# Performance work log

Hardware: AMD Instinct MI355X
Metric: run time of the kernel (lower is better)

Reference implementation:

```python
import jax, jax.numpy as jnp
import numpy as np

D_MODEL = 1024
N_HEAD = 16
HEAD_DIM = D_MODEL // N_HEAD
N_POS = 4096
K_PROJ = 256  # self.k is hardcoded to 256 in the module
BATCH = 4


def setup_inputs() -> dict:
    key = jax.random.key(0)
    ks = jax.random.split(key, 11)
    s = 1.0 / np.sqrt(D_MODEL)
    return {
        "x": jax.random.normal(ks[0], (BATCH, N_POS, D_MODEL), jnp.float32),
        "Wq": jax.random.normal(ks[1], (D_MODEL, D_MODEL), jnp.float32) * s,
        "bq": jnp.zeros((D_MODEL,), jnp.float32),
        "Wk": jax.random.normal(ks[2], (D_MODEL, D_MODEL), jnp.float32) * s,
        "bk": jnp.zeros((D_MODEL,), jnp.float32),
        "Wv": jax.random.normal(ks[3], (D_MODEL, D_MODEL), jnp.float32) * s,
        "bv": jnp.zeros((D_MODEL,), jnp.float32),
        "E": jax.random.normal(ks[4], (K_PROJ, N_POS), jnp.float32),
        "F": jax.random.normal(ks[5], (K_PROJ, N_POS), jnp.float32),
        "Wo": jax.random.normal(ks[6], (D_MODEL, D_MODEL), jnp.float32) * s,
        "bo": jnp.zeros((D_MODEL,), jnp.float32),
    }


def reference(x, Wq, bq, Wk, bk, Wv, bv, E, F, Wo, bo):
    B, N, D = x.shape
    scale = jnp.sqrt(jnp.asarray(HEAD_DIM, x.dtype))
    # Q/K/V projections (nn.Linear applies x @ W.T + b)
    def proj(W, b):
        y = jnp.einsum('bnd,ed->bne', x, W) + b
        return y.reshape(B, N, N_HEAD, HEAD_DIM).transpose(0, 2, 1, 3)  # bhnd
    Q = proj(Wq, bq)
    K = proj(Wk, bk)
    V = proj(Wv, bv)
    # Linformer low-rank projections along sequence dim
    Kp = jnp.einsum('kn,bhnd->bhkd', E, K)
    Vp = jnp.einsum('kn,bhnd->bhkd', F, V)
    attn_score = jnp.einsum('bhnd,bhkd->bhnk', Q, Kp) / scale
    attn = jax.nn.softmax(attn_score, axis=-1)  # dropout is identity (drop_prob=0)
    out = jnp.einsum('bhnk,bhkd->bhnd', attn, Vp)
    out = out.transpose(0, 2, 1, 3).reshape(B, N, D)
    out = jnp.einsum('bnd,ed->bne', out, Wo) + bo
    return out, attn_score
```

## Files before the change

### kernel.cpp

```cpp
#include <hip/hip_runtime.h>

typedef _Float16 f16;
typedef __attribute__((ext_vector_type(8))) _Float16 f16x8;
typedef __attribute__((ext_vector_type(4))) _Float16 f16x4;
typedef __attribute__((ext_vector_type(4))) float f32x4;

typedef const __attribute__((address_space(1))) unsigned int* gas_ptr;
typedef __attribute__((address_space(3))) unsigned int* las_ptr;

__device__ __forceinline__ void gload16(const f16* g, f16* l) {
  __builtin_amdgcn_global_load_lds((gas_ptr)g, (las_ptr)l, 16, 0, 0);
}

template<int WM, int WN, bool OUT32>
__device__ __forceinline__ void gemm_core(
    const f16* __restrict__ A, int lda,
    const f16* __restrict__ B, int ldb,
    int kLen,
    f16* lsA, f16* lsB,
    float* __restrict__ C32, f16* __restrict__ C16, int ldc,
    float scale, const float* __restrict__ biasC, const float* __restrict__ biasR)
{
  constexpr int T   = WM * WN * 64;
  constexpr int nA  = (WM * 64 * 8) / T;
  constexpr int nB  = (WN * 64 * 8) / T;
  constexpr int RPI = T / 8;
  const int t    = threadIdx.x;
  const int lane = t & 63;
  const int wave = t >> 6;
  const int wm   = wave / WN;
  const int wn   = wave % WN;

  f32x4 acc[4][4];
  const f32x4 z4 = {0.f, 0.f, 0.f, 0.f};
#pragma unroll
  for (int i = 0; i < 4; ++i)
#pragma unroll
    for (int j = 0; j < 4; ++j) acc[i][j] = z4;

  const int r_ = t >> 3;
  const int c_ = (t & 7) * 8;
  const int ldsOff = (wave << 9);

  for (int kt = 0; kt < kLen; kt += 64) {
#pragma unroll
    for (int i = 0; i < nA; ++i) {
      const f16* g = A + (size_t)(i * RPI + r_) * lda + kt + c_;
      gload16(g, lsA + i * (T * 8) + ldsOff);
    }
#pragma unroll
    for (int i = 0; i < nB; ++i) {
      const f16* g = B + (size_t)(i * RPI + r_) * ldb + kt + c_;
      gload16(g, lsB + i * (T * 8) + ldsOff);
    }
    __syncthreads();
#pragma unroll
    for (int ks = 0; ks < 2; ++ks) {
      f16x8 af[4], bf[4];
#pragma unroll
      for (int i = 0; i < 4; ++i)
        af[i] = *(const f16x8*)&lsA[(wm * 64 + i * 16 + (lane & 15)) * 64 + ks * 32 + (lane >> 4) * 8];
#pragma unroll
      for (int j = 0; j < 4; ++j)
        bf[j] = *(const f16x8*)&lsB[(wn * 64 + j * 16 + (lane & 15)) * 64 + ks * 32 + (lane >> 4) * 8];
#pragma unroll
      for (int i = 0; i < 4; ++i)
#pragma unroll
        for (int j = 0; j < 4; ++j)
          acc[i][j] = __builtin_amdgcn_mfma_f32_16x16x32_f16(af[i], bf[j], acc[i][j], 0, 0, 0);
    }
    __syncthreads();
  }

  const int lc = lane & 15;
  const int lr = (lane >> 4) * 4;
#pragma unroll
  for (int j = 0; j < 4; ++j) {
    const int col = wn * 64 + j * 16 + lc;
    const float bC = biasC ? biasC[col] : 0.f;
#pragma unroll
    for (int i = 0; i < 4; ++i) {
      const int rbase = wm * 64 + i * 16 + lr;
#pragma unroll
      for (int r = 0; r < 4; ++r) {
        const int row = rbase + r;
        float v = acc[i][j][r] * scale + bC;
        if (biasR) v += biasR[row];
        if (OUT32) C32[(size_t)row * ldc + col] = v;
        else       C16[(size_t)row * ldc + col] = (f16)v;
      }
    }
  }
}

template<int WM, int WN, bool OUT32>
__global__ __launch_bounds__(WM * WN * 64) void k_gemm(
    const f16* A, int lda, const f16* B, int ldb, int kLen,
    float* C32, f16* C16, int ldc, float scale,
    const float* biasC, const float* biasR)
{
  __shared__ f16 lsA[WM * 64 * 64];
  __shared__ f16 lsB[WN * 64 * 64];
  const size_t rt = blockIdx.y, ct = blockIdx.x;
  gemm_core<WM, WN, OUT32>(
      A + rt * (WM * 64) * (size_t)lda, lda,
      B + ct * (WN * 64) * (size_t)ldb, ldb, kLen,
      lsA, lsB,
      OUT32 ? C32 + rt * (WM * 64) * (size_t)ldc + ct * (WN * 64) : nullptr,
      OUT32 ? nullptr : C16 + rt * (WM * 64) * (size_t)ldc + ct * (WN * 64), ldc,
      scale,
      biasC ? biasC + ct * (WN * 64) : nullptr,
      biasR ? biasR + rt * (WM * 64) : nullptr);
}

__global__ __launch_bounds__(256) void k_cast_xt(const float* __restrict__ x,
                                                 f16* __restrict__ Xf,
                                                 f16* __restrict__ XT)
{
  __shared__ f16 tile[64][68];
  const int b = blockIdx.z, bi = blockIdx.y, bj = blockIdx.x;
  const int r0 = threadIdx.x >> 4;
  const int c4 = (threadIdx.x & 15) * 4;
  const float* xb = x + ((size_t)b * 4096 + (size_t)bi * 64) * 1024 + bj * 64;
#pragma unroll
  for (int rr = 0; rr < 4; ++rr) {
    const int row = rr * 16 + r0;
    const float4 v = *(const float4*)(xb + (size_t)row * 1024 + c4);
    f16x4 h = {(f16)v.x, (f16)v.y, (f16)v.z, (f16)v.w};
    *(f16x4*)&tile[row][c4] = h;
    *(f16x4*)(Xf + ((size_t)b * 4096 + (size_t)bi * 64 + row) * 1024 + bj * 64 + c4) = h;
  }
  __syncthreads();
#pragma unroll
  for (int rr = 0; rr < 4; ++rr) {
    const int col = rr * 16 + r0;
    f16x4 h = {tile[c4 + 0][col], tile[c4 + 1][col], tile[c4 + 2][col], tile[c4 + 3][col]};
    *(f16x4*)(XT + ((size_t)b * 1024 + (size_t)bj * 64 + col) * 4096 + (size_t)bi * 64 + c4) = h;
  }
}

__global__ __launch_bounds__(256) void k_cast_w(
    const float* w0, const float* w1, const float* w2,
    const float* w3, const float* w4, const float* w5, f16* __restrict__ d)
{
  const size_t i = ((size_t)blockIdx.x * 256 + threadIdx.x) * 4;
  const int seg = (int)(i >> 20);
  const float* s = (seg == 0) ? w0 : (seg == 1) ? w1 : (seg == 2) ? w2
                 : (seg == 3) ? w3 : (seg == 4) ? w4 : w5;
  const float4 v = *(const float4*)(s + (i & 1048575));
  f16x4 o = {(f16)v.x, (f16)v.y, (f16)v.z, (f16)v.w};
  *(f16x4*)(d + i) = o;
}

__global__ __launch_bounds__(256) void k_rowsum(const float* __restrict__ E,
                                                const float* __restrict__ F,
                                                float* __restrict__ rs)
{
  const int r = blockIdx.x * 4 + (threadIdx.x >> 6);
  const int lane = threadIdx.x & 63;
  const float* src = (r < 256) ? (E + (size_t)r * 4096) : (F + (size_t)(r - 256) * 4096);
  float s = 0.f;
#pragma unroll
  for (int i = 0; i < 16; ++i) {
    const float4 v = *(const float4*)(src + i * 256 + lane * 4);
    s += v.x + v.y + v.z + v.w;
  }
#pragma unroll
  for (int o = 32; o; o >>= 1) s += __shfl_xor(s, o);
  if (lane == 0) rs[r] = s;
}

__global__ __launch_bounds__(256) void k_exfx(const f16* __restrict__ EF,
                                              const f16* __restrict__ XT,
                                              float* __restrict__ part)
{
  __shared__ f16 lsA[128 * 64];
  __shared__ f16 lsB[128 * 64];
  const int z = blockIdx.z; const int b = z & 3; const int s = z >> 2;
  const int rt = blockIdx.y, ct = blockIdx.x;
  const f16* A = EF + (size_t)rt * 128 * 4096 + s * 1024;
  const f16* B = XT + (size_t)b * 1024 * 4096 + (size_t)ct * 128 * 4096 + s * 1024;
  float* C = part + (size_t)z * (512 * 1024) + (size_t)rt * 128 * 1024 + ct * 128;
  gemm_core<2, 2, true>(A, 4096, B, 4096, 1024, lsA, lsB, C, nullptr, 1024, 1.f, nullptr, nullptr);
}

__global__ __launch_bounds__(256) void k_reduce2(const float* __restrict__ part,
                                                 f16* __restrict__ EXf)
{
  const size_t i = ((size_t)blockIdx.x * 256 + threadIdx.x) * 4;
  const size_t b = i >> 19;
  const size_t idx = i & 524287;
  const float4 a = *(const float4*)(part + (0 * 4 + b) * 524288 + idx);
  const float4 c1 = *(const float4*)(part + (1 * 4 + b) * 524288 + idx);
  const float4 c2 = *(const float4*)(part + (2 * 4 + b) * 524288 + idx);
  const float4 c3 = *(const float4*)(part + (3 * 4 + b) * 524288 + idx);
  f16x4 o = {(f16)(a.x + c1.x + c2.x + c3.x), (f16)(a.y + c1.y + c2.y + c3.y),
             (f16)(a.z + c1.z + c2.z + c3.z), (f16)(a.w + c1.w + c2.w + c3.w)};
  *(f16x4*)(EXf + i) = o;
}

__global__ __launch_bounds__(256) void k_kpvp(const f16* __restrict__ EXf,
                                              const f16* __restrict__ W16,
                                              float* __restrict__ p2)
{
  __shared__ f16 lsA[128 * 64];
  __shared__ f16 lsB[128 * 64];
  const int z = blockIdx.z; const int which = z & 1; const int s = z >> 1;
  const int rt = blockIdx.y, ct = blockIdx.x;
  const f16 *A, *B;
  if (which == 0) {
    const int b = rt >> 1, r0 = (rt & 1) * 128;
    A = EXf + ((size_t)b * 512 + r0) * 1024 + s * 512;
    B = W16 + 1048576 + (size_t)ct * 128 * 1024 + s * 512;
  } else {
    const int b = ct >> 1, r0 = (ct & 1) * 128;
    A = W16 + 2 * 1048576 + (size_t)rt * 128 * 1024 + s * 512;
    B = EXf + ((size_t)b * 512 + 256 + r0) * 1024 + s * 512;
  }
  float* C = p2 + (size_t)(s * 2 + which) * 1048576 + (size_t)rt * 128 * 1024 + ct * 128;
  gemm_core<2, 2, true>(A, 1024, B, 1024, 512, lsA, lsB, C, nullptr, 1024, 1.f, nullptr, nullptr);
}

__global__ __launch_bounds__(256) void k_reduce3(const float* __restrict__ p2,
                                                 f16* __restrict__ KpVp,
                                                 const float* __restrict__ rs,
                                                 const float* __restrict__ bk,
                                                 const float* __restrict__ bv)
{
  const size_t i = ((size_t)blockIdx.x * 256 + threadIdx.x) * 4;
  const int half = (int)(i >> 20);
  const size_t j = i & 1048575;
  size_t pidx; float r1[4];
  if (half == 0) {
    const int r  = (int)((j >> 10) & 255);
    const int hd = (int)(j & 1023);
    pidx = j;
    const float se = rs[r];
#pragma unroll
    for (int t = 0; t < 4; ++t) r1[t] = se * bk[hd + t];
  } else {
    const int b  = (int)(j >> 18);
    const int hd = (int)((j >> 8) & 1023);
    const int r  = (int)(j & 255);
    pidx = (size_t)hd * 1024 + (size_t)b * 256 + r;
    const float bb = bv[hd];
#pragma unroll
    for (int t = 0; t < 4; ++t) r1[t] = bb * rs[256 + r + t];
  }
  const float4 a = *(const float4*)(p2 + (size_t)(0 * 2 + half) * 1048576 + pidx);
  const float4 c = *(const float4*)(p2 + (size_t)(1 * 2 + half) * 1048576 + pidx);
  f16x4 o = {(f16)(a.x + c.x + r1[0]), (f16)(a.y + c.y + r1[1]),
             (f16)(a.z + c.z + r1[2]), (f16)(a.w + c.w + r1[3])};
  *(f16x4*)(KpVp + i) = o;
}

__global__ __launch_bounds__(256) void k_attn(const f16* __restrict__ Q,
                                              const f16* __restrict__ Kp,
                                              const f16* __restrict__ VpT,
                                              float* __restrict__ S,
                                              f16* __restrict__ OP)
{
  __shared__ char smem[98304];
  f16* lsK = (f16*)smem;
  f16* lsQ = (f16*)(smem + 32768);
  f16* lsV = (f16*)(smem + 65536);

  const int rt = blockIdx.x, h = blockIdx.y, b = blockIdx.z;
  const int t = threadIdx.x, lane = t & 63, w = t >> 6;
  const int g = lane >> 4;
  const int c = lane & 15;

  const int r_ = t >> 3;
  const int cswz = ((t & 7) * 16) ^ ((r_ & 7) << 4);
  const char* Kg = (const char*)(Kp + (size_t)b * 262144 + h * 64);
  const char* Qg = (const char*)(Q + ((size_t)b * 4096 + (size_t)rt * 128) * 1024 + h * 64);
#pragma unroll
  for (int i = 0; i < 8; ++i)
    gload16((const f16*)(Kg + (size_t)(i * 32 + r_) * 2048 + cswz),
            lsK + i * 2048 + (w << 9));
#pragma unroll
  for (int i = 0; i < 4; ++i)
    gload16((const f16*)(Qg + (size_t)(i * 32 + r_) * 2048 + cswz),
            lsQ + i * 2048 + (w << 9));
  {
    const char* Vb = (const char*)(VpT + ((size_t)b * 1024 + h * 64) * 256);
    const int vrow = lane >> 5;
    const int voff = (lane & 31) * 16;
#pragma unroll
    for (int i = 0; i < 8; ++i) {
      const int row = i * 8 + w * 2 + vrow;
      const int so = voff ^ ((row & 7) << 4);
      gload16((const f16*)(Vb + (size_t)row * 512 + so),
              (f16*)((char*)lsV + i * 4096 + w * 1024));
    }
  }
  __syncthreads();

  const int swz = (lane & 7) << 4;
  f32x4 acc[16][2];
  const f32x4 z4 = {0.f, 0.f, 0.f, 0.f};
#pragma unroll
  for (int i = 0; i < 16; ++i) { acc[i][0] = z4; acc[i][1] = z4; }
#pragma unroll
  for (int ks = 0; ks < 2; ++ks) {
    const int koff = ks * 64 + g * 16;
    f16x8 bf[2];
#pragma unroll
    for (int j = 0; j < 2; ++j) {
      const int row = w * 32 + j * 16 + c;
      bf[j] = *(const f16x8*)((const char*)lsQ + row * 128 + (koff ^ swz));
    }
#pragma unroll
    for (int i = 0; i < 16; ++i) {
      const f16x8 af = *(const f16x8*)((const char*)lsK + (i * 16 + c) * 128 + (koff ^ swz));
      acc[i][0] = __builtin_amdgcn_mfma_f32_16x16x32_f16(af, bf[0], acc[i][0], 0, 0, 0);
      acc[i][1] = __builtin_amdgcn_mfma_f32_16x16x32_f16(af, bf[1], acc[i][1], 0, 0, 0);
    }
  }

  float* Sb = S + (((size_t)(b * 16 + h)) * 4096 + (size_t)rt * 128 + w * 32) * 256;
#pragma unroll
  for (int j = 0; j < 2; ++j)
#pragma unroll
    for (int i = 0; i < 16; ++i) {
      acc[i][j] *= 0.125f;
      *(f32x4*)(Sb + (size_t)(j * 16 + c) * 256 + i * 16 + g * 4) = acc[i][j];
    }

  float pinv[2];
#pragma unroll
  for (int j = 0; j < 2; ++j) {
    float m = acc[0][j][0];
#pragma unroll
    for (int i = 0; i < 16; ++i)
      m = fmaxf(m, fmaxf(fmaxf(acc[i][j][0], acc[i][j][1]),
                         fmaxf(acc[i][j][2], acc[i][j][3])));
    m = fmaxf(m, __shfl_xor(m, 16));
    m = fmaxf(m, __shfl_xor(m, 32));
    float s = 0.f;
#pragma unroll
    for (int i = 0; i < 16; ++i)
#pragma unroll
      for (int r2 = 0; r2 < 4; ++r2) {
        const float e = __expf(acc[i][j][r2] - m);
        acc[i][j][r2] = e;
        s += e;
      }
    s += __shfl_xor(s, 16);
    s += __shfl_xor(s, 32);
    pinv[j] = 1.f / s;
  }

  __syncthreads();
  char* lsP = (char*)smem;
#pragma unroll
  for (int j = 0; j < 2; ++j) {
    const int n = w * 32 + j * 16 + c;
    char* base = lsP + n * 512;
#pragma unroll
    for (int i = 0; i < 16; ++i) {
      f16x4 p = {(f16)(acc[i][j][0] * pinv[j]), (f16)(acc[i][j][1] * pinv[j]),
                 (f16)(acc[i][j][2] * pinv[j]), (f16)(acc[i][j][3] * pinv[j])};
      *(f16x4*)(base + ((i * 32 + g * 8) ^ swz)) = p;
    }
  }
  __syncthreads();

  f32x4 o[2][4];
#pragma unroll
  for (int i2 = 0; i2 < 2; ++i2)
#pragma unroll
    for (int jh = 0; jh < 4; ++jh) o[i2][jh] = z4;
#pragma unroll
  for (int ks = 0; ks < 8; ++ks) {
    const int koff = ks * 64 + g * 16;
    f16x8 pa[2];
#pragma unroll
    for (int i2 = 0; i2 < 2; ++i2) {
      const int n = w * 32 + i2 * 16 + c;
      pa[i2] = *(const f16x8*)(lsP + n * 512 + (koff ^ swz));
    }
#pragma unroll
    for (int jh = 0; jh < 4; ++jh) {
      const f16x8 vb = *(const f16x8*)((const char*)lsV + (jh * 16 + c) * 512 + (koff ^ swz));
      o[0][jh] = __builtin_amdgcn_mfma_f32_16x16x32_f16(pa[0], vb, o[0][jh], 0, 0, 0);
      o[1][jh] = __builtin_amdgcn_mfma_f32_16x16x32_f16(pa[1], vb, o[1][jh], 0, 0, 0);
    }
  }

  f16* Ob = OP + ((size_t)b * 4096 + (size_t)rt * 128 + w * 32) * 1024 + h * 64;
#pragma unroll
  for (int jh = 0; jh < 4; ++jh) {
    const int col = jh * 16 + c;
#pragma unroll
    for (int i2 = 0; i2 < 2; ++i2) {
      const int rb = i2 * 16 + g * 4;
#pragma unroll
      for (int r2 = 0; r2 < 4; ++r2)
        Ob[(size_t)(rb + r2) * 1024 + col] = (f16)o[i2][jh][r2];
    }
  }
}

extern "C" void kernel_launch(void* const* d_in, const int* in_sizes, int n_in,
                              void* d_out, int out_size, void* d_ws, size_t ws_size,
                              hipStream_t stream) {
  const float* x  = (const float*)d_in[0];
  const float* Wq = (const float*)d_in[1];
  const float* bq = (const float*)d_in[2];
  const float* Wk = (const float*)d_in[3];
  const float* bk = (const float*)d_in[4];
  const float* Wv = (const float*)d_in[5];
  const float* bv = (const float*)d_in[6];
  const float* E  = (const float*)d_in[7];
  const float* F  = (const float*)d_in[8];
  const float* Wo = (const float*)d_in[9];
  const float* bo = (const float*)d_in[10];

  float* out = (float*)d_out;
  float* S   = out + 16777216;

  char* w = (char*)d_ws;
  f16*   Xf     = (f16*)w;
  f16*   EXf    = (f16*)w;
  float* rowsum = (float*)(w + 4 * 1048576);
  f16*   XT     = (f16*)(w + 33554432);
  f16*   OPf    = (f16*)(w + 33554432);
  f16*   Qf     = (f16*)(w + (size_t)2 * 33554432);
  float* part   = (float*)(w + (size_t)3 * 33554432);
  float* part2  = (float*)(w + (size_t)3 * 33554432);
  f16*   W16    = (f16*)(w + (size_t)4 * 33554432);
  f16*   EF16   = W16 + (size_t)4 * 1048576;
  f16*   KpVp   = (f16*)(w + (size_t)4 * 33554432 + 12582912);

  k_cast_xt<<<dim3(16, 64, 4), 256, 0, stream>>>(x, Xf, XT);
  k_cast_w<<<6144, 256, 0, stream>>>(Wq, Wk, Wv, Wo, E, F, W16);

  k_gemm<2, 2, false><<<dim3(8, 128), 256, 0, stream>>>(
      Xf, 1024, W16, 1024, 1024, nullptr, Qf, 1024, 1.f, bq, nullptr);

  k_rowsum<<<128, 256, 0, stream>>>(E, F, rowsum);

  k_exfx<<<dim3(8, 4, 16), 256, 0, stream>>>(EF16, XT, part);
  k_reduce2<<<2048, 256, 0, stream>>>(part, EXf);

  k_kpvp<<<dim3(8, 8, 4), 256, 0, stream>>>(EXf, W16, part2);
  k_reduce3<<<2048, 256, 0, stream>>>(part2, KpVp, rowsum, bk, bv);

  k_attn<<<dim3(32, 16, 4), 256, 0, stream>>>(
      Qf, KpVp, KpVp + (size_t)4 * 262144, S, OPf);

  k_gemm<2, 2, true><<<dim3(8, 128), 256, 0, stream>>>(
      OPf, 1024, W16 + 3 * 1048576, 1024, 1024, out, nullptr, 1024, 1.f, bo, nullptr);
}
```

Measured before the change: 654.2 us.

## Add 256x256-tile pipelined GEMM for Q and output projections

```diff
diff --git a/kernel.cpp b/kernel.cpp
--- a/kernel.cpp
+++ b/kernel.cpp
@@ -88,6 +88,114 @@
         if (biasR) v += biasR[row];
         if (OUT32) C32[(size_t)row * ldc + col] = v;
         else       C16[(size_t)row * ldc + col] = (f16)v;
+      }
+    }
+  }
+}
+
+template<bool OUT32>
+__global__ __launch_bounds__(512) void k_gemm256(
+    const f16* __restrict__ A, int lda,
+    const f16* __restrict__ B, int ldb,
+    int kLen, int nct,
+    float* __restrict__ C32, f16* __restrict__ C16, int ldc,
+    const float* __restrict__ biasC)
+{
+  __shared__ f16 ls[4][2][8192];
+
+  const int cpx = gridDim.x >> 3;
+  const int wg  = (blockIdx.x & 7) * cpx + (blockIdx.x >> 3);
+  const int rt  = wg / nct, ct = wg % nct;
+
+  const int t    = threadIdx.x;
+  const int lane = t & 63;
+  const int w    = t >> 6;
+  const int wm   = w >> 2;
+  const int wn   = w & 3;
+  const int c    = lane & 15;
+  const int g    = lane >> 4;
+  const int ch   = c >> 1;
+  const int c1   = c & 1;
+  const int jsw  = (g ^ (ch & 3)) << 4;
+
+  const f16* Ab = A + (size_t)rt * 256 * lda;
+  const f16* Bb = B + (size_t)ct * 256 * ldb;
+
+  const int srow = ((t >> 3) << 1) + ((t >> 2) & 1);
+  const int sj   = ((t & 3) ^ ((t >> 3) & 3)) * 8;
+  const int NT   = kLen >> 5;
+
+#define STAGE_A(tile) { const int kt_ = (tile) * 32; f16* d_ = &ls[(tile) & 3][0][0]; \
+    gload16(Ab + (size_t)srow * lda + kt_ + sj, d_ + t * 8); \
+    gload16(Ab + (size_t)(srow + 128) * lda + kt_ + sj, d_ + 4096 + t * 8); }
+#define STAGE_B(tile) { const int kt_ = (tile) * 32; f16* d_ = &ls[(tile) & 3][1][0]; \
+    gload16(Bb + (size_t)srow * ldb + kt_ + sj, d_ + t * 8); \
+    gload16(Bb + (size_t)(srow + 128) * ldb + kt_ + sj, d_ + 4096 + t * 8); }
+
+  STAGE_A(0); STAGE_B(0);
+  STAGE_A(1); STAGE_B(1);
+  asm volatile("s_waitcnt vmcnt(4)" ::: "memory");
+  __builtin_amdgcn_s_barrier();
+
+  f32x4 acc[8][4];
+  const f32x4 z4 = {0.f, 0.f, 0.f, 0.f};
+#pragma unroll
+  for (int i = 0; i < 8; ++i)
+#pragma unroll
+    for (int j = 0; j < 4; ++j) acc[i][j] = z4;
+
+  for (int tt = 0; tt < NT; ++tt) {
+    const char* lA = (const char*)&ls[tt & 3][0][0];
+    const char* lB = (const char*)&ls[tt & 3][1][0];
+    f16x8 af[8], bf[4];
+#pragma unroll
+    for (int mf = 0; mf < 4; ++mf)
+      af[mf] = *(const f16x8*)(lA + (size_t)(wm * 64 + mf * 8 + ch) * 128 + c1 * 64 + jsw);
+#pragma unroll
+    for (int nf = 0; nf < 4; ++nf)
+      bf[nf] = *(const f16x8*)(lB + (size_t)(wn * 32 + nf * 8 + ch) * 128 + c1 * 64 + jsw);
+    if (tt + 2 < NT) STAGE_A(tt + 2);
+    __builtin_amdgcn_s_barrier();
+    __builtin_amdgcn_s_setprio(1);
+#pragma unroll
+    for (int mf = 0; mf < 4; ++mf)
+#pragma unroll
+      for (int nf = 0; nf < 4; ++nf)
+        acc[mf][nf] = __builtin_amdgcn_mfma_f32_16x16x32_f16(af[mf], bf[nf], acc[mf][nf], 0, 0, 0);
+    __builtin_amdgcn_s_setprio(0);
+#pragma unroll
+    for (int mf = 4; mf < 8; ++mf)
+      af[mf] = *(const f16x8*)(lA + (size_t)(wm * 64 + mf * 8 + ch) * 128 + c1 * 64 + jsw);
+    if (tt + 2 < NT) {
+      STAGE_B(tt + 2);
+      asm volatile("s_waitcnt vmcnt(4)" ::: "memory");
+    } else {
+      asm volatile("s_waitcnt vmcnt(0)" ::: "memory");
+    }
+    __builtin_amdgcn_s_barrier();
+    __builtin_amdgcn_s_setprio(1);
+#pragma unroll
+    for (int mf = 4; mf < 8; ++mf)
+#pragma unroll
+      for (int nf = 0; nf < 4; ++nf)
+        acc[mf][nf] = __builtin_amdgcn_mfma_f32_16x16x32_f16(af[mf], bf[nf], acc[mf][nf], 0, 0, 0);
+    __builtin_amdgcn_s_setprio(0);
+  }
+#undef STAGE_A
+#undef STAGE_B
+
+#pragma unroll
+  for (int nf = 0; nf < 4; ++nf) {
+    const int col = ct * 256 + wn * 64 + nf * 16 + c;
+    const float bC = biasC ? biasC[col] : 0.f;
+#pragma unroll
+    for (int mf = 0; mf < 8; ++mf) {
+      const int rbase = rt * 256 + wm * 128 + mf * 16 + g * 4;
+#pragma unroll
+      for (int r = 0; r < 4; ++r) {
+        const float v = acc[mf][nf][r] + bC;
+        if (OUT32) __builtin_nontemporal_store(v, C32 + (size_t)(rbase + r) * ldc + col);
+        else       C16[(size_t)(rbase + r) * ldc + col] = (f16)v;
       }
     }
   }
@@ -324,7 +432,8 @@
 #pragma unroll
     for (int i = 0; i < 16; ++i) {
       acc[i][j] *= 0.125f;
-      *(f32x4*)(Sb + (size_t)(j * 16 + c) * 256 + i * 16 + g * 4) = acc[i][j];
+      __builtin_nontemporal_store(acc[i][j],
+          (f32x4*)(Sb + (size_t)(j * 16 + c) * 256 + i * 16 + g * 4));
     }
 
   float pinv[2];
@@ -436,8 +545,8 @@
   k_cast_xt<<<dim3(16, 64, 4), 256, 0, stream>>>(x, Xf, XT);
   k_cast_w<<<6144, 256, 0, stream>>>(Wq, Wk, Wv, Wo, E, F, W16);
 
-  k_gemm<2, 2, false><<<dim3(8, 128), 256, 0, stream>>>(
-      Xf, 1024, W16, 1024, 1024, nullptr, Qf, 1024, 1.f, bq, nullptr);
+  k_gemm256<false><<<256, 512, 0, stream>>>(
+      Xf, 1024, W16, 1024, 1024, 4, nullptr, Qf, 1024, bq);
 
   k_rowsum<<<128, 256, 0, stream>>>(E, F, rowsum);
 
@@ -450,6 +559,6 @@
   k_attn<<<dim3(32, 16, 4), 256, 0, stream>>>(
       Qf, KpVp, KpVp + (size_t)4 * 262144, S, OPf);
 
-  k_gemm<2, 2, true><<<dim3(8, 128), 256, 0, stream>>>(
-      OPf, 1024, W16 + 3 * 1048576, 1024, 1024, out, nullptr, 1024, 1.f, bo, nullptr);
-}
+  k_gemm256<true><<<256, 512, 0, stream>>>(
+      OPf, 1024, W16 + 3 * 1048576, 1024, 1024, 4, out, nullptr, 1024, bo);
+}
```

After: 599.5 us. 8.4% less time.
